# Kernel tuning notes

Measured on AMD Instinct MI355X. Metric: run time of the kernel, lower is better.

Reference implementation:

```python
import jax, jax.numpy as jnp
import numpy as np

BS, TS, NA, OS = 32, 256, 16, 512
HID, D, W = 1024, 128, 8            # sw_hidden_dim, sw_input_dim, sw_window_size
OUT, DEC, NACT = 512, 512, 30       # sw_output_dim, sw_decoder_hidden_layer, n_actions


def setup_inputs() -> dict:
    key = jax.random.key(0)
    ks = jax.random.split(key, 12)
    p = lambda k, shape: jax.random.normal(k, shape, jnp.float32) * 0.02
    return {
        "inputs": jax.random.normal(ks[0], (BS, TS, NA, OS), jnp.float32),
        "hidden_state": jnp.zeros((BS, NA, (W - 1) * D), jnp.float32),
        "w1": p(ks[1], (OS, HID)),        "b1": jnp.zeros((HID,), jnp.float32),
        "w2": p(ks[2], (HID, D)),         "b2": jnp.zeros((D,), jnp.float32),
        "w3": p(ks[3], (W * D, OUT)),     "b3": jnp.zeros((OUT,), jnp.float32),
        "w4": p(ks[4], (OUT, DEC)),       "b4": jnp.zeros((DEC,), jnp.float32),
        "w5": p(ks[5], (DEC, NACT)),      "b5": jnp.zeros((NACT,), jnp.float32),
    }


def reference(inputs, hidden_state, w1, b1, w2, b2, w3, b3, w4, b4, w5, b5):
    bs, ts, na, _ = inputs.shape
    # encoder: two pointwise MLP layers over (bs, ts, na, *)
    x = jax.nn.relu(inputs @ w1 + b1)          # (bs, ts, na, HID)
    x = jax.nn.relu(x @ w2 + b2)               # (bs, ts, na, D)
    # build the full frame sequence: W-1 hidden frames followed by ts encoded frames
    hid_frames = hidden_state.reshape(bs, na, W - 1, D)
    seq = jnp.concatenate([hid_frames, jnp.transpose(x, (0, 2, 1, 3))], axis=2)  # (bs, na, ts+W-1, D)
    # sliding windows: window at step t = frames [t, t+W) — vectorized over all t
    wins = jnp.stack([seq[:, :, i:i + ts, :] for i in range(W)], axis=3)  # (bs, na, ts, W, D)
    wins = wins.reshape(bs, na, ts, W * D)
    h = jax.nn.relu(wins @ w3 + b3)            # (bs, na, ts, OUT)
    h = jnp.transpose(h, (0, 2, 1, 3))         # (bs, ts, na, OUT)
    h = jax.nn.relu(h @ w4 + b4)               # (bs, ts, na, DEC)
    q = h @ w5 + b5                            # (bs, ts, na, NACT)
    # final carried window: last W-1 frames of the sequence, flattened per agent
    window = seq[:, :, ts:, :].reshape(bs, na, (W - 1) * D)
    return (q, window)
```

## Files before the change

kernel.cpp:

```cpp
#include <hip/hip_runtime.h>
#include <hip/hip_bf16.h>
#include <hip/hip_fp8.h>


#define DEVI __device__ __forceinline__

typedef float f32x4 __attribute__((ext_vector_type(4)));
typedef short s16x8 __attribute__((ext_vector_type(8)));
typedef short s16x4 __attribute__((ext_vector_type(4)));
typedef long long i64;
typedef unsigned long long u64;

#define ROWS 131072
#define SEQ_T 263

#define W2P_OFF 524288
#define W3P_OFF 655360
#define W4P_OFF 1179648
#define W5P_OFF 1441792
#define WP_TOTAL 1458176

#define W3P8_BYTE_OFF 2916352
#define SEQ8_BYTE_OFF 3440640
#define W4P8_BYTE_OFF 20971520
#define BIG_BYTE_OFF 37388288

DEVI short f2bf(float f) {
  union { __hip_bfloat16 h; short s; } u;
  u.h = __float2bfloat16(f);
  return u.s;
}
DEVI float bf2f(short s) {
  union { float f; unsigned int u; } v;
  v.u = ((unsigned int)(unsigned short)s) << 16;
  return v.f;
}

DEVI unsigned int f2e4(float f) {
  union { __hip_fp8_e4m3 h; unsigned char c; } u;
  u.h = __hip_fp8_e4m3(f);
  return (unsigned int)u.c;
}

#if __has_builtin(__builtin_amdgcn_cvt_pk_fp8_f32)
DEVI unsigned int pk4e4(float a, float b, float c, float d) {
  int v = 0;
  v = __builtin_amdgcn_cvt_pk_fp8_f32(a, b, v, false);
  v = __builtin_amdgcn_cvt_pk_fp8_f32(c, d, v, true);
  return (unsigned int)v;
}
#else
DEVI unsigned int pk4e4(float a, float b, float c, float d) {
  return f2e4(a) | (f2e4(b) << 8) | (f2e4(c) << 16) | (f2e4(d) << 24);
}
#endif

DEVI f32x4 MFMA(s16x8 a, s16x8 b, f32x4 c) {
  return __builtin_amdgcn_mfma_f32_16x16x32_bf16(a, b, c, 0, 0, 0);
}
DEVI f32x4 MFMA8(i64 a, i64 b, f32x4 c) {
  return __builtin_amdgcn_mfma_f32_16x16x32_fp8_fp8(a, b, c, 0, 0, 0);
}

__global__ __launch_bounds__(256) void pack_w_kernel(
    const float* __restrict__ w1, const float* __restrict__ w2,
    const float* __restrict__ w3, const float* __restrict__ w4,
    const float* __restrict__ w5, short* __restrict__ wp)
{
  int idx = blockIdx.x * 256 + threadIdx.x;
  const float* src; int sh, Nsrc, local;
  if (idx < W2P_OFF)      { src = w1; sh = 4; Nsrc = 1024; local = idx; }
  else if (idx < W3P_OFF) { src = w2; sh = 5; Nsrc = 128;  local = idx - W2P_OFF; }
  else if (idx < W4P_OFF) { src = w3; sh = 5; Nsrc = 512;  local = idx - W3P_OFF; }
  else if (idx < W5P_OFF) { src = w4; sh = 4; Nsrc = 512;  local = idx - W4P_OFF; }
  else                    { src = w5; sh = 4; Nsrc = 30;   local = idx - W5P_OFF; }
  int j    = local & 7;
  int lane = (local >> 3) & 63;
  int rest = local >> 9;
  int k0   = rest & ((1 << sh) - 1);
  int n0   = rest >> sh;
  int k = (k0 << 5) + ((lane >> 4) << 3) + j;
  int n = (n0 << 4) + (lane & 15);
  float v = (n < Nsrc) ? src[k * Nsrc + n] : 0.f;
  wp[idx] = f2bf(v);
}

__global__ __launch_bounds__(256) void pack_w_fp8_kernel(
    const float* __restrict__ w1, const float* __restrict__ w2,
    const float* __restrict__ w3, const float* __restrict__ w4,
    unsigned char* __restrict__ wp8, unsigned char* __restrict__ w3p8,
    unsigned char* __restrict__ w4p8)
{
  int t = blockIdx.x * 256 + threadIdx.x;
  const float* src; int nkshift, Nsrc, dt; unsigned char* dst;
  if (t < 65536)       { src = w1; dt = t;          nkshift = 4; Nsrc = 1024; dst = wp8; }
  else if (t < 81920)  { src = w2; dt = t - 65536;  nkshift = 5; Nsrc = 128;  dst = wp8 + 524288; }
  else if (t < 147456) { src = w3; dt = t - 81920;  nkshift = 5; Nsrc = 512;  dst = w3p8; }
  else                 { src = w4; dt = t - 147456; nkshift = 4; Nsrc = 512;  dst = w4p8; }
  int lane = dt & 63;
  int rest = dt >> 6;
  int k0   = rest & ((1 << nkshift) - 1);
  int n0   = rest >> nkshift;
  int kb = (k0 << 5) + ((lane >> 4) << 3);
  int n  = (n0 << 4) + (lane & 15);
  float v[8];
  #pragma unroll
  for (int j = 0; j < 8; ++j) v[j] = src[(kb + j) * Nsrc + n];
  u64 pk = (u64)pk4e4(v[0], v[1], v[2], v[3])
         | ((u64)pk4e4(v[4], v[5], v[6], v[7]) << 32);
  *(u64*)(dst + (long)dt * 8) = pk;
}

__global__ __launch_bounds__(256) void hid_copy_kernel(
    const float* __restrict__ hid, unsigned char* __restrict__ seq8)
{
  int t = blockIdx.x * 256 + threadIdx.x;
  int j = t & 15;
  int r = t >> 4;
  int i = r % 7;
  int ba = r / 7;
  int s = j ^ i;
  const float* src = hid + (r << 7) + (j << 3);
  f32x4 a = *(const f32x4*)src;
  f32x4 b = *(const f32x4*)(src + 4);
  u64 pk = (u64)pk4e4(a[0], a[1], a[2], a[3])
         | ((u64)pk4e4(b[0], b[1], b[2], b[3]) << 32);
  *(u64*)(seq8 + (ba * SEQ_T + i) * 128 + s * 8) = pk;
}

__global__ __launch_bounds__(512, 4) void enc_kernel(
    const float* __restrict__ inp, const unsigned char* __restrict__ w1p8,
    const float* __restrict__ b1, const unsigned char* __restrict__ w2p8,
    const float* __restrict__ b2, unsigned char* __restrict__ seq8)
{
  __shared__ unsigned char As8[32768] __attribute__((aligned(16)));
  __shared__ unsigned char h1q8[16384] __attribute__((aligned(16)));
  const int tid = threadIdx.x;
  const int lane = tid & 63, wv = tid >> 6;
  const int l15 = lane & 15, lg = lane >> 4;
  const int rb = blockIdx.x << 6;

  #pragma unroll
  for (int it = 0; it < 8; ++it) {
    int g = it * 512 + tid;
    int row = g >> 6, j = g & 63;
    const float* s = inp + (long)(rb + row) * 512 + j * 8;
    f32x4 v0 = *(const f32x4*)s;
    f32x4 v1 = *(const f32x4*)(s + 4);
    u64 pk = (u64)pk4e4(v0[0], v0[1], v0[2], v0[3])
           | ((u64)pk4e4(v1[0], v1[1], v1[2], v1[3]) << 32);
    *(u64*)(As8 + (j << 9) + ((row ^ (j & 7)) << 3)) = pk;
  }
  __syncthreads();

  f32x4 z = {0.f, 0.f, 0.f, 0.f};
  f32x4 acc2[4] = {z, z, z, z};

  for (int p = 0; p < 4; ++p) {
    f32x4 acc1[2][4];
    #pragma unroll
    for (int i = 0; i < 2; ++i)
      #pragma unroll
      for (int j = 0; j < 4; ++j) acc1[i][j] = z;

    const unsigned char* wB = w1p8 + (((p * 16 + wv * 2) * 16) << 9) + lane * 8;

    i64 Wc[2];
    Wc[0] = *(const i64*)(wB);
    Wc[1] = *(const i64*)(wB + (16 << 9));

    #pragma unroll 1
    for (int k0 = 0; k0 < 16; ++k0) {
      int kn = (k0 + 1) & 15;
      i64 Wn0 = *(const i64*)(wB + (kn << 9));
      i64 Wn1 = *(const i64*)(wB + ((16 + kn) << 9));
      int k2 = k0 * 4 + lg;
      int c = k2 & 7;
      i64 Xc[4];
      #pragma unroll
      for (int mi = 0; mi < 4; ++mi)
        Xc[mi] = *(const i64*)(As8 + (k2 << 9) + (((mi * 16 + l15) ^ c) << 3));
      #pragma unroll
      for (int mi = 0; mi < 4; ++mi) {
        acc1[0][mi] = MFMA8(Wc[0], Xc[mi], acc1[0][mi]);
        acc1[1][mi] = MFMA8(Wc[1], Xc[mi], acc1[1][mi]);
      }
      Wc[0] = Wn0; Wc[1] = Wn1;
    }
    __syncthreads();
    #pragma unroll
    for (int ci = 0; ci < 2; ++ci) {
      f32x4 bv = *(const f32x4*)(b1 + p * 256 + wv * 32 + ci * 16 + lg * 4);
      int k2c = wv * 4 + ci * 2 + (lg >> 1);
      int half = (lg & 1) << 2;
      #pragma unroll
      for (int mi = 0; mi < 4; ++mi) {
        int m = mi * 16 + l15;
        unsigned int pk = pk4e4(fmaxf(acc1[ci][mi][0] + bv[0], 0.f),
                                fmaxf(acc1[ci][mi][1] + bv[1], 0.f),
                                fmaxf(acc1[ci][mi][2] + bv[2], 0.f),
                                fmaxf(acc1[ci][mi][3] + bv[3], 0.f));
        *(unsigned int*)(h1q8 + (k2c << 9) + (m << 3) + half) = pk;
      }
    }
    __syncthreads();
    const unsigned char* w2B = w2p8 + ((wv * 32 + p * 8) << 9) + lane * 8;
    i64 W2c = *(const i64*)(w2B);
    #pragma unroll 1
    for (int kk = 0; kk < 8; ++kk) {
      int kn = (kk + 1) & 7;
      i64 W2n = *(const i64*)(w2B + (kn << 9));
      i64 X2[4];
      #pragma unroll
      for (int mi = 0; mi < 4; ++mi)
        X2[mi] = *(const i64*)(h1q8 + ((kk * 4 + lg) << 9) + ((mi * 16 + l15) << 3));
      #pragma unroll
      for (int mi = 0; mi < 4; ++mi)
        acc2[mi] = MFMA8(W2c, X2[mi], acc2[mi]);
      W2c = W2n;
    }
  }
  __syncthreads();
  unsigned char* scr8 = As8;
  {
    f32x4 bv = *(const f32x4*)(b2 + wv * 16 + lg * 4);
    int gsb = wv * 2 + (lg >> 1);
    int off4 = (lg & 1) << 2;
    #pragma unroll
    for (int mi = 0; mi < 4; ++mi) {
      int m = mi * 16 + l15;
      int f7 = ((rb >> 4) + mi + 7) & 7;
      unsigned int pk = pk4e4(fmaxf(acc2[mi][0] + bv[0], 0.f),
                              fmaxf(acc2[mi][1] + bv[1], 0.f),
                              fmaxf(acc2[mi][2] + bv[2], 0.f),
                              fmaxf(acc2[mi][3] + bv[3], 0.f));
      int ls = (gsb ^ f7) ^ (m & 7);
      *(unsigned int*)(scr8 + m * 128 + ls * 8 + off4) = pk;
    }
  }
  __syncthreads();
  #pragma unroll
  for (int it = 0; it < 2; ++it) {
    int c = it * 512 + tid;
    int i = c >> 4, s = c & 15;
    u64 v = *(const u64*)(scr8 + i * 128 + ((s ^ (i & 7)) << 3));
    int r = rb + i;
    int ba2 = ((r >> 12) << 4) + (r & 15);
    int t = (r >> 4) & 255;
    int f = t + 7;
    *(u64*)(seq8 + (ba2 * SEQ_T + f) * 128 + (s << 3)) = v;
  }
}

__global__ __launch_bounds__(256) void enc_hi_kernel(
    const float* __restrict__ inp, const short* __restrict__ w1p,
    const float* __restrict__ b1, const short* __restrict__ w2p,
    const float* __restrict__ b2, float* __restrict__ out)
{
  __shared__ short As[8192]  __attribute__((aligned(16)));
  __shared__ short h1s[16384] __attribute__((aligned(16)));
  const int tid = threadIdx.x;
  const int lane = tid & 63, wv = tid >> 6;
  const int l15 = lane & 15, lg = lane >> 4;
  const int b = blockIdx.x / 7, ti = blockIdx.x % 7;
  const int t = 249 + ti;
  const long row0 = (long)b * 4096 + t * 16;

  #pragma unroll
  for (int it = 0; it < 4; ++it) {
    int c = it * 256 + tid;
    int m = c >> 6, j = c & 63;
    const float* s = inp + (row0 + m) * 512 + j * 8;
    f32x4 v0 = *(const f32x4*)s;
    f32x4 v1 = *(const f32x4*)(s + 4);
    s16x8 o;
    o[0]=f2bf(v0[0]); o[1]=f2bf(v0[1]); o[2]=f2bf(v0[2]); o[3]=f2bf(v0[3]);
    o[4]=f2bf(v1[0]); o[5]=f2bf(v1[1]); o[6]=f2bf(v1[2]); o[7]=f2bf(v1[3]);
    *(s16x8*)((char*)As + (j << 8) + (((m ^ (j & 15)) & 15) << 4)) = o;
  }
  __syncthreads();

  f32x4 z = {0.f, 0.f, 0.f, 0.f};
  f32x4 acc1[16];
  #pragma unroll
  for (int i = 0; i < 16; ++i) acc1[i] = z;
  #pragma unroll 1
  for (int k0 = 0; k0 < 16; ++k0) {
    int k2 = k0 * 4 + lg;
    s16x8 X = *(const s16x8*)((const char*)As + (k2 << 8) + (((l15 ^ (k2 & 15)) & 15) << 4));
    #pragma unroll
    for (int ci = 0; ci < 16; ++ci) {
      s16x8 W = *(const s16x8*)(w1p + (((wv * 16 + ci) * 16 + k0) << 9) + lane * 8);
      acc1[ci] = MFMA(W, X, acc1[ci]);
    }
  }
  #pragma unroll
  for (int ci = 0; ci < 16; ++ci) {
    f32x4 bv = *(const f32x4*)(b1 + wv * 256 + ci * 16 + lg * 4);
    int k2c = wv * 32 + ci * 2 + (lg >> 1);
    int half = (lg & 1) << 3;
    s16x4 o;
    #pragma unroll
    for (int j = 0; j < 4; ++j)
      o[j] = f2bf(fmaxf(acc1[ci][j] + bv[j], 0.f));
    *(s16x4*)((char*)h1s + (k2c << 8) + (l15 << 4) + half) = o;
  }
  __syncthreads();
  f32x4 acc2[2] = {z, z};
  #pragma unroll 1
  for (int kk = 0; kk < 32; ++kk) {
    s16x8 X2 = *(const s16x8*)((const char*)h1s + ((kk * 4 + lg) << 8) + (l15 << 4));
    #pragma unroll
    for (int nf = 0; nf < 2; ++nf) {
      s16x8 W2 = *(const s16x8*)(w2p + (((wv * 2 + nf) * 32 + kk) << 9) + lane * 8);
      acc2[nf] = MFMA(W2, X2, acc2[nf]);
    }
  }
  #pragma unroll
  for (int nf = 0; nf < 2; ++nf) {
    #pragma unroll
    for (int rr = 0; rr < 4; ++rr) {
      int d = (wv * 2 + nf) * 16 + lg * 4 + rr;
      float v = fmaxf(acc2[nf][rr] + b2[d], 0.f);
      out[3932160 + (((b * 16 + l15) * 7 + ti) << 7) + d] = v;
    }
  }
}

__global__ __launch_bounds__(512, 4) void win_kernel(
    const unsigned char* __restrict__ seq8, const unsigned char* __restrict__ w3p8,
    const float* __restrict__ b3, unsigned char* __restrict__ h3p8)
{
  __shared__ unsigned char sh8[17280] __attribute__((aligned(16)));
  __shared__ short rp[16384] __attribute__((aligned(16)));
  const int tid = threadIdx.x;
  const int lane = tid & 63, wid = tid >> 6;
  const int wm = wid >> 2, wn = wid & 3;
  const int l15 = lane & 15, lg = lane >> 4;
  const int bid = blockIdx.x;
  const int th = bid & 1, ba = bid >> 1;
  const int t0 = th << 7;

  const unsigned char* gsrc = seq8 + (ba * SEQ_T + t0) * 128;
  #pragma unroll
  for (int i = 0; i < 3; ++i) {
    int c = i * 512 + tid;
    if (c < 1080) *(s16x8*)&sh8[c * 16] = *(const s16x8*)(gsrc + c * 16);
  }
  __syncthreads();

  f32x4 z = {0.f, 0.f, 0.f, 0.f};
  for (int h = 0; h < 2; ++h) {
    f32x4 acc[4][4];
    #pragma unroll
    for (int i = 0; i < 4; ++i)
      #pragma unroll
      for (int j = 0; j < 4; ++j) acc[i][j] = z;

    const unsigned char* bB = w3p8 + (((h * 16 + wn * 4) * 32) << 9) + lane * 8;
    i64 bcur[4];
    #pragma unroll
    for (int nf = 0; nf < 4; ++nf) bcur[nf] = *(const i64*)(bB + ((nf * 32) << 9));

    #pragma unroll 1
    for (int kc = 0; kc < 32; ++kc) {
      int kn = (kc + 1) & 31;
      i64 bnxt[4];
      #pragma unroll
      for (int nf = 0; nf < 4; ++nf) bnxt[nf] = *(const i64*)(bB + ((nf * 32 + kn) << 9));
      int w = kc >> 2;
      int dslot = ((kc & 3) << 2) + lg;
      i64 av[4];
      #pragma unroll
      for (int mf = 0; mf < 4; ++mf) {
        int f = wm * 64 + mf * 16 + l15 + w;
        av[mf] = *(const i64*)(sh8 + f * 128 + ((dslot ^ (f & 7)) << 3));
      }
      #pragma unroll
      for (int nf = 0; nf < 4; ++nf)
        #pragma unroll
        for (int mf = 0; mf < 4; ++mf)
          acc[mf][nf] = MFMA8(av[mf], bcur[nf], acc[mf][nf]);
      #pragma unroll
      for (int nf = 0; nf < 4; ++nf) bcur[nf] = bnxt[nf];
    }

    for (int s = 0; s < 2; ++s) {
      __syncthreads();
      #pragma unroll
      for (int mf = 0; mf < 4; ++mf)
        #pragma unroll
        for (int e = 0; e < 2; ++e) {
          int nf = s * 2 + e;
          float bias = b3[h * 256 + wn * 64 + nf * 16 + l15];
          int lc = wn * 32 + e * 16 + l15;
          #pragma unroll
          for (int rr = 0; rr < 4; ++rr) {
            int row = wm * 64 + mf * 16 + lg * 4 + rr;
            float v = fmaxf(acc[mf][nf][rr] + bias, 0.f);
            int by = ((row << 8) + (lc << 1)) ^ ((row & 7) << 4);
            rp[by >> 1] = f2bf(v);
          }
        }
      __syncthreads();
      #pragma unroll
      for (int it = 0; it < 4; ++it) {
        int c = it * 512 + tid;
        int cl = c & 15, g = (c >> 4) & 3, wni = (c >> 6) & 3, tt = (c >> 8) & 7;
        int row = tt * 16 + cl;
        int lc = wni * 32 + g * 8;
        int by = ((row << 8) + (lc << 1)) ^ ((row & 7) << 4);
        s16x8 v = *(const s16x8*)((const char*)rp + by);
        u64 pk = (u64)pk4e4(bf2f(v[0]), bf2f(v[1]), bf2f(v[2]), bf2f(v[3]))
               | ((u64)pk4e4(bf2f(v[4]), bf2f(v[5]), bf2f(v[6]), bf2f(v[7])) << 32);
        int k0g = h * 8 + wni * 2 + s;
        int mt = ba * 16 + th * 8 + tt;
        long dst = ((long)((mt * 16 + k0g) * 64 + g * 16 + cl)) << 3;
        *(u64*)(h3p8 + dst) = pk;
      }
    }
  }
}

__global__ __launch_bounds__(512, 4) void dec_kernel(
    const unsigned char* __restrict__ h3p8, const unsigned char* __restrict__ w4p8,
    const float* __restrict__ b4, const short* __restrict__ w5p,
    const float* __restrict__ b5, float* __restrict__ out)
{
  __shared__ short h4s[32768] __attribute__((aligned(16)));
  const int tid = threadIdx.x;
  const int lane = tid & 63, wid = tid >> 6;
  const int wm = wid >> 2, wn = wid & 3;
  const int mf5 = wid;
  const int l15 = lane & 15, lg = lane >> 4;
  const int rb = blockIdx.x << 7;

  f32x4 z = {0.f, 0.f, 0.f, 0.f};
  f32x4 acc5[2] = {z, z};
  const unsigned char* aBase = h3p8 + (long)((rb >> 4) + wm * 4) * 8192 + lane * 8;

  for (int h = 0; h < 2; ++h) {
    f32x4 acc[4][4];
    #pragma unroll
    for (int i = 0; i < 4; ++i)
      #pragma unroll
      for (int j = 0; j < 4; ++j) acc[i][j] = z;

    const unsigned char* bB = w4p8 + (((h * 16 + wn * 4) * 16) << 9) + lane * 8;
    i64 bcur[4];
    #pragma unroll
    for (int nf = 0; nf < 4; ++nf) bcur[nf] = *(const i64*)(bB + ((nf * 16) << 9));

    #pragma unroll 1
    for (int k0 = 0; k0 < 16; ++k0) {
      int kn = (k0 + 1) & 15;
      i64 bnxt[4];
      #pragma unroll
      for (int nf = 0; nf < 4; ++nf) bnxt[nf] = *(const i64*)(bB + ((nf * 16 + kn) << 9));
      i64 av[4];
      #pragma unroll
      for (int mf = 0; mf < 4; ++mf) av[mf] = *(const i64*)(aBase + mf * 8192 + k0 * 512);
      #pragma unroll
      for (int nf = 0; nf < 4; ++nf)
        #pragma unroll
        for (int mf = 0; mf < 4; ++mf)
          acc[mf][nf] = MFMA8(av[mf], bcur[nf], acc[mf][nf]);
      #pragma unroll
      for (int nf = 0; nf < 4; ++nf) bcur[nf] = bnxt[nf];
    }
    __syncthreads();
    #pragma unroll
    for (int mf = 0; mf < 4; ++mf)
      #pragma unroll
      for (int nf = 0; nf < 4; ++nf) {
        int lc = wn * 64 + nf * 16 + l15;
        float bias = b4[h * 256 + lc];
        #pragma unroll
        for (int rr = 0; rr < 4; ++rr) {
          int row = wm * 64 + mf * 16 + lg * 4 + rr;
          float v = fmaxf(acc[mf][nf][rr] + bias, 0.f);
          int by = ((row << 9) + (lc << 1)) ^ ((row & 7) << 4);
          h4s[by >> 1] = f2bf(v);
        }
      }
    __syncthreads();
    #pragma unroll
    for (int kk = 0; kk < 8; ++kk) {
      int row = mf5 * 16 + l15;
      int by = ((row << 9) + (kk << 6) + (lg << 4)) ^ ((row & 7) << 4);
      s16x8 a0 = *(const s16x8*)((const char*)h4s + by);
      #pragma unroll
      for (int nf = 0; nf < 2; ++nf) {
        s16x8 wb = *(const s16x8*)(w5p + (nf * 16 + h * 8 + kk) * 512 + lane * 8);
        acc5[nf] = MFMA(a0, wb, acc5[nf]);
      }
    }
  }
  #pragma unroll
  for (int nf = 0; nf < 2; ++nf) {
    int col = nf * 16 + l15;
    if (col < 30) {
      float bias = b5[col];
      #pragma unroll
      for (int rr = 0; rr < 4; ++rr) {
        int row_ = rb + mf5 * 16 + lg * 4 + rr;
        int t = row_ & 255;
        int ba2 = row_ >> 8;
        int orow = (((ba2 >> 4) << 8) + t) * 16 + (ba2 & 15);
        out[orow * 30 + col] = acc5[nf][rr] + bias;
      }
    }
  }
}

extern "C" void kernel_launch(void* const* d_in, const int* in_sizes, int n_in,
                              void* d_out, int out_size, void* d_ws, size_t ws_size,
                              hipStream_t stream) {
  const float* inp = (const float*)d_in[0];
  const float* hid = (const float*)d_in[1];
  const float* w1  = (const float*)d_in[2];
  const float* b1  = (const float*)d_in[3];
  const float* w2  = (const float*)d_in[4];
  const float* b2  = (const float*)d_in[5];
  const float* w3  = (const float*)d_in[6];
  const float* b3  = (const float*)d_in[7];
  const float* w4  = (const float*)d_in[8];
  const float* b4  = (const float*)d_in[9];
  const float* w5  = (const float*)d_in[10];
  const float* b5  = (const float*)d_in[11];

  char* ws = (char*)d_ws;
  short* wp   = (short*)ws;
  short* w1p  = wp;
  short* w2p  = wp + W2P_OFF;
  short* w5p  = wp + W5P_OFF;
  unsigned char* w3p8 = (unsigned char*)(ws + W3P8_BYTE_OFF);
  unsigned char* seq8 = (unsigned char*)(ws + SEQ8_BYTE_OFF);
  unsigned char* w4p8 = (unsigned char*)(ws + W4P8_BYTE_OFF);
  unsigned char* h3p8 = (unsigned char*)(ws + BIG_BYTE_OFF);
  unsigned char* w1p8 = h3p8;
  unsigned char* w2p8 = w1p8 + 524288;
  float* out  = (float*)d_out;

  pack_w_kernel    <<<WP_TOTAL / 256, 256, 0, stream>>>(w1, w2, w3, w4, w5, wp);
  pack_w_fp8_kernel<<<704, 256, 0, stream>>>(w1, w2, w3, w4, w1p8, w3p8, w4p8);
  hid_copy_kernel  <<<224, 256, 0, stream>>>(hid, seq8);
  enc_kernel       <<<2048, 512, 0, stream>>>(inp, w1p8, b1, w2p8, b2, seq8);
  enc_hi_kernel    <<<224, 256, 0, stream>>>(inp, w1p, b1, w2p, b2, out);
  win_kernel       <<<1024, 512, 0, stream>>>(seq8, w3p8, b3, h3p8);
  dec_kernel       <<<1024, 512, 0, stream>>>(h3p8, w4p8, b4, w5p, b5, out);
}
```

Measured before the change: 471.1 us.

## Widen encoder hidden chunk to 512 and drop unused bf16 w3/w4 packing

The encoder kernel now processes the 1024-wide hidden layer in two passes of 512 columns instead of four passes of 256. Each wave holds four weight column tiles per step, so every A-fragment load from LDS feeds more MFMAs, and there are half as many barrier-separated phases. The h1 staging buffer doubles to 32 KB, which raises LDS use and accumulator registers and may reduce occupancy. Separately, the bf16 weight packing kernel stops converting w3 and w4, which nothing reads, shrinking that launch.

After: 446.4 us. -5.2%, faster.

```diff
diff --git a/kernel.cpp b/kernel.cpp
--- a/kernel.cpp
+++ b/kernel.cpp
@@ -15,10 +15,8 @@
 #define SEQ_T 263
 
 #define W2P_OFF 524288
-#define W3P_OFF 655360
-#define W4P_OFF 1179648
 #define W5P_OFF 1441792
-#define WP_TOTAL 1458176
+#define PACKW_TOTAL 671744
 
 #define W3P8_BYTE_OFF 2916352
 #define SEQ8_BYTE_OFF 3440640
@@ -64,16 +62,13 @@
 
 __global__ __launch_bounds__(256) void pack_w_kernel(
     const float* __restrict__ w1, const float* __restrict__ w2,
-    const float* __restrict__ w3, const float* __restrict__ w4,
     const float* __restrict__ w5, short* __restrict__ wp)
 {
   int idx = blockIdx.x * 256 + threadIdx.x;
-  const float* src; int sh, Nsrc, local;
-  if (idx < W2P_OFF)      { src = w1; sh = 4; Nsrc = 1024; local = idx; }
-  else if (idx < W3P_OFF) { src = w2; sh = 5; Nsrc = 128;  local = idx - W2P_OFF; }
-  else if (idx < W4P_OFF) { src = w3; sh = 5; Nsrc = 512;  local = idx - W3P_OFF; }
-  else if (idx < W5P_OFF) { src = w4; sh = 4; Nsrc = 512;  local = idx - W4P_OFF; }
-  else                    { src = w5; sh = 4; Nsrc = 30;   local = idx - W5P_OFF; }
+  const float* src; int sh, Nsrc, local; long dsto;
+  if (idx < W2P_OFF)     { src = w1; sh = 4; Nsrc = 1024; local = idx;          dsto = idx; }
+  else if (idx < 655360) { src = w2; sh = 5; Nsrc = 128;  local = idx - W2P_OFF; dsto = idx; }
+  else                   { src = w5; sh = 4; Nsrc = 30;   local = idx - 655360;  dsto = W5P_OFF + (idx - 655360); }
   int j    = local & 7;
   int lane = (local >> 3) & 63;
   int rest = local >> 9;
@@ -82,7 +77,7 @@
   int k = (k0 << 5) + ((lane >> 4) << 3) + j;
   int n = (n0 << 4) + (lane & 15);
   float v = (n < Nsrc) ? src[k * Nsrc + n] : 0.f;
-  wp[idx] = f2bf(v);
+  wp[dsto] = f2bf(v);
 }
 
 __global__ __launch_bounds__(256) void pack_w_fp8_kernel(
@@ -134,7 +129,7 @@
     const float* __restrict__ b2, unsigned char* __restrict__ seq8)
 {
   __shared__ unsigned char As8[32768] __attribute__((aligned(16)));
-  __shared__ unsigned char h1q8[16384] __attribute__((aligned(16)));
+  __shared__ unsigned char h1q8[32768] __attribute__((aligned(16)));
   const int tid = threadIdx.x;
   const int lane = tid & 63, wv = tid >> 6;
   const int l15 = lane & 15, lg = lane >> 4;
@@ -156,24 +151,25 @@
   f32x4 z = {0.f, 0.f, 0.f, 0.f};
   f32x4 acc2[4] = {z, z, z, z};
 
-  for (int p = 0; p < 4; ++p) {
-    f32x4 acc1[2][4];
-    #pragma unroll
-    for (int i = 0; i < 2; ++i)
+  for (int p = 0; p < 2; ++p) {
+    f32x4 acc1[4][4];
+    #pragma unroll
+    for (int i = 0; i < 4; ++i)
       #pragma unroll
       for (int j = 0; j < 4; ++j) acc1[i][j] = z;
 
-    const unsigned char* wB = w1p8 + (((p * 16 + wv * 2) * 16) << 9) + lane * 8;
-
-    i64 Wc[2];
-    Wc[0] = *(const i64*)(wB);
-    Wc[1] = *(const i64*)(wB + (16 << 9));
+    const unsigned char* wB = w1p8 + (((p * 32 + wv * 4) * 16) << 9) + lane * 8;
+
+    i64 Wc[4];
+    #pragma unroll
+    for (int ci = 0; ci < 4; ++ci) Wc[ci] = *(const i64*)(wB + ((ci * 16) << 9));
 
     #pragma unroll 1
     for (int k0 = 0; k0 < 16; ++k0) {
       int kn = (k0 + 1) & 15;
-      i64 Wn0 = *(const i64*)(wB + (kn << 9));
-      i64 Wn1 = *(const i64*)(wB + ((16 + kn) << 9));
+      i64 Wn[4];
+      #pragma unroll
+      for (int ci = 0; ci < 4; ++ci) Wn[ci] = *(const i64*)(wB + ((ci * 16 + kn) << 9));
       int k2 = k0 * 4 + lg;
       int c = k2 & 7;
       i64 Xc[4];
@@ -181,17 +177,18 @@
       for (int mi = 0; mi < 4; ++mi)
         Xc[mi] = *(const i64*)(As8 + (k2 << 9) + (((mi * 16 + l15) ^ c) << 3));
       #pragma unroll
-      for (int mi = 0; mi < 4; ++mi) {
-        acc1[0][mi] = MFMA8(Wc[0], Xc[mi], acc1[0][mi]);
-        acc1[1][mi] = MFMA8(Wc[1], Xc[mi], acc1[1][mi]);
-      }
-      Wc[0] = Wn0; Wc[1] = Wn1;
+      for (int ci = 0; ci < 4; ++ci)
+        #pragma unroll
+        for (int mi = 0; mi < 4; ++mi)
+          acc1[ci][mi] = MFMA8(Wc[ci], Xc[mi], acc1[ci][mi]);
+      #pragma unroll
+      for (int ci = 0; ci < 4; ++ci) Wc[ci] = Wn[ci];
     }
     __syncthreads();
     #pragma unroll
-    for (int ci = 0; ci < 2; ++ci) {
-      f32x4 bv = *(const f32x4*)(b1 + p * 256 + wv * 32 + ci * 16 + lg * 4);
-      int k2c = wv * 4 + ci * 2 + (lg >> 1);
+    for (int ci = 0; ci < 4; ++ci) {
+      f32x4 bv = *(const f32x4*)(b1 + p * 512 + wv * 64 + ci * 16 + lg * 4);
+      int k2c = wv * 8 + ci * 2 + (lg >> 1);
       int half = (lg & 1) << 2;
       #pragma unroll
       for (int mi = 0; mi < 4; ++mi) {
@@ -204,11 +201,11 @@
       }
     }
     __syncthreads();
-    const unsigned char* w2B = w2p8 + ((wv * 32 + p * 8) << 9) + lane * 8;
+    const unsigned char* w2B = w2p8 + ((wv * 32 + p * 16) << 9) + lane * 8;
     i64 W2c = *(const i64*)(w2B);
     #pragma unroll 1
-    for (int kk = 0; kk < 8; ++kk) {
-      int kn = (kk + 1) & 7;
+    for (int kk = 0; kk < 16; ++kk) {
+      int kn = (kk + 1) & 15;
       i64 W2n = *(const i64*)(w2B + (kn << 9));
       i64 X2[4];
       #pragma unroll
@@ -542,7 +539,7 @@
   unsigned char* w2p8 = w1p8 + 524288;
   float* out  = (float*)d_out;
 
-  pack_w_kernel    <<<WP_TOTAL / 256, 256, 0, stream>>>(w1, w2, w3, w4, w5, wp);
+  pack_w_kernel    <<<PACKW_TOTAL / 256, 256, 0, stream>>>(w1, w2, w5, wp);
   pack_w_fp8_kernel<<<704, 256, 0, stream>>>(w1, w2, w3, w4, w1p8, w3p8, w4p8);
   hid_copy_kernel  <<<224, 256, 0, stream>>>(hid, seq8);
   enc_kernel       <<<2048, 512, 0, stream>>>(inp, w1p8, b1, w2p8, b2, seq8);
```
